# Kernel optimization log

Measured on AMD Instinct MI355X. Metric: run time of the kernel, lower is better.

## Reference

```python
import jax, jax.numpy as jnp
import numpy as np

R, S, H, L = 4096, 64, 256, 3  # rays, samples/ray, mlp width, n hidden-to-hidden layers
FAR_DELTA = 1e10


def setup_inputs() -> dict:
    key = jax.random.key(0)
    ks = jax.random.split(key, 16)
    points = jax.random.normal(ks[0], (R, S, 3), dtype=jnp.float32)
    dirs = jax.random.normal(ks[1], (R, S, 3), dtype=jnp.float32)
    dirs = dirs / jnp.linalg.norm(dirs, axis=-1, keepdims=True)
    # sorted depths in a [2, 6] near/far range (monotone along sample axis)
    z_vals = jnp.sort(2.0 + 4.0 * jax.random.uniform(ks[2], (R, S), dtype=jnp.float32), axis=-1)
    time = jax.random.uniform(ks[3], (R, S), dtype=jnp.float32)

    def w(k, shape):
        return 0.05 * jax.random.normal(k, shape, dtype=jnp.float32)

    return {
        'points': points, 'dirs': dirs, 'z_vals': z_vals, 'time': time,
        'sW_in': w(ks[4], (6, H)),  'sb_in': jnp.zeros((H,), jnp.float32),
        'sW_h':  w(ks[5], (L, H, H)), 'sb_h': jnp.zeros((L, H), jnp.float32),
        'sW_out': w(ks[6], (H, 4)), 'sb_out': jnp.zeros((4,), jnp.float32),
        'dW_in': w(ks[7], (7, H)),  'db_in': jnp.zeros((H,), jnp.float32),
        'dW_h':  w(ks[8], (L, H, H)), 'db_h': jnp.zeros((L, H), jnp.float32),
        'dW_out': w(ks[9], (H, 5)), 'db_out': jnp.zeros((5,), jnp.float32),
    }


def _mlp(x, W_in, b_in, W_h, b_h, W_out, b_out):
    h = jax.nn.relu(x @ W_in + b_in)
    for i in range(W_h.shape[0]):  # fixed small layer count
        h = jax.nn.relu(h @ W_h[i] + b_h[i])
    return h @ W_out + b_out


def _compute_weights(sigma, z_vals):
    delta = z_vals[..., 1:] - z_vals[..., :-1]
    delta = jnp.concatenate([delta, jnp.full_like(delta[..., :1], FAR_DELTA)], axis=-1)
    alpha = 1.0 - jnp.exp(-sigma * delta)
    trans = jnp.cumprod(
        jnp.concatenate([jnp.ones_like(alpha[..., :1]), 1.0 - alpha + 1e-10], axis=-1),
        axis=-1)[..., :-1]
    return alpha * trans


def reference(points, dirs, z_vals, time,
              sW_in, sb_in, sW_h, sb_h, sW_out, sb_out,
              dW_in, db_in, dW_h, db_h, dW_out, db_out):
    static_out = _mlp(jnp.concatenate([points, dirs], axis=-1),
                      sW_in, sb_in, sW_h, sb_h, sW_out, sb_out)          # [R,S,4]
    dynamic_out = _mlp(jnp.concatenate([points, dirs, time[..., None]], axis=-1),
                       dW_in, db_in, dW_h, db_h, dW_out, db_out)         # [R,S,5]

    static_sigma = static_out[..., 0]
    static_rgb = jax.nn.sigmoid(static_out[..., 1:4])
    dynamic_sigma = dynamic_out[..., 0]
    dynamic_rgb = jax.nn.sigmoid(dynamic_out[..., 1:4])
    bw = jax.nn.sigmoid(dynamic_out[..., 4])                             # [R,S]

    sigma = (1.0 - bw) * static_sigma + bw * dynamic_sigma               # [R,S]
    rgb = (1.0 - bw)[..., None] * static_rgb + bw[..., None] * dynamic_rgb  # [R,S,3]

    weights = _compute_weights(sigma, z_vals)                            # [R,S]
    rgb_map = jnp.sum(weights[..., None] * rgb, axis=-2)                 # [R,3]
    depth_map = jnp.sum(weights * z_vals, axis=-1)                       # [R]
    return (rgb_map, depth_map, weights, (1.0 - bw) * weights, bw * weights)
```

## Files before the change

kernel.cpp:

```cpp
#include <hip/hip_runtime.h>

#define R_ 4096
#define S_ 64
#define H_ 256
#define N_ (R_ * S_)
#define FARD 1e10f

typedef __attribute__((ext_vector_type(4))) float f32x4;
typedef __attribute__((ext_vector_type(8))) short short8;
typedef __attribute__((ext_vector_type(8))) int i32x8;

union U8 { short8 s; uint4 u; };
union V8 { i32x8 v; uint4 q[2]; };

__device__ __forceinline__ unsigned int cvt_pk_bf16(float lo, float hi) {
    unsigned int r;
    asm("v_cvt_pk_bf16_f32 %0, %1, %2" : "=v"(r) : "v"(lo), "v"(hi));
    return r;
}
__device__ __forceinline__ unsigned short f2bf(float f) {
    unsigned int x = __float_as_uint(f);
    x += 0x7fffu + ((x >> 16) & 1u);
    return (unsigned short)(x >> 16);
}
__device__ __forceinline__ unsigned int pk4_fp8(float a0, float a1, float a2, float a3) {
    unsigned int lo, hi;
    asm("v_cvt_pk_fp8_f32 %0, %1, %2" : "=v"(lo) : "v"(a0), "v"(a1));
    asm("v_cvt_pk_fp8_f32 %0, %1, %2" : "=v"(hi) : "v"(a2), "v"(a3));
    return (lo & 0xffffu) | (hi << 16);
}
__device__ __forceinline__ unsigned char f2fp8(float v) {
    unsigned int r;
    asm("v_cvt_pk_fp8_f32 %0, %1, %2" : "=v"(r) : "v"(v), "v"(0.0f));
    return (unsigned char)(r & 0xff);
}
__device__ __forceinline__ float sigmoidf_(float x) { return 1.0f / (1.0f + expf(-x)); }

typedef const __attribute__((address_space(1))) unsigned char* gas1;
typedef __attribute__((address_space(3))) unsigned char* las3;
__device__ __forceinline__ void stage64k(const unsigned char* g, unsigned char* l, int tid) {
#pragma unroll
    for (int i = 0; i < 8; ++i)
        __builtin_amdgcn_global_load_lds((gas1)(g + i * 8192 + tid * 16),
                                         (las3)(l + i * 8192 + tid * 16), 16, 0, 0);
}


__device__ __forceinline__ void store_act_frag(unsigned char* act, const unsigned int pk[8],
                                               int lane, int wv)
{
    const int m0 = lane & 15;
    const int q  = lane >> 4;
    const int sp = wv >> 2;
    const int c4 = (wv & 3) << 4;
#pragma unroll
    for (int nt = 0; nt < 2; ++nt)
#pragma unroll
        for (int mt = 0; mt < 4; ++mt)
            *(unsigned int*)(act + (mt * 2 + sp) * 2048 + nt * 1024 +
                             (c4 + m0) * 16 + 4 * q) = pk[nt * 4 + mt];
}

__device__ void hidden_layer(unsigned char* act, unsigned char* wbuf,
                             const unsigned char* __restrict__ next_panel,
                             const float* __restrict__ bias, int lane, int wv, int tid)
{
    const int m0 = lane & 15;
    const int q  = lane >> 4;
    const int nw = wv << 5;

    f32x4 acc[2][4];
#pragma unroll
    for (int nt = 0; nt < 2; ++nt) {
        const float4 bv = *(const float4*)&bias[nw + nt * 16 + 4 * q];
#pragma unroll
        for (int mt = 0; mt < 4; ++mt) {
            acc[nt][mt][0] = bv.x; acc[nt][mt][1] = bv.y;
            acc[nt][mt][2] = bv.z; acc[nt][mt][3] = bv.w;
        }
    }

    __builtin_amdgcn_s_setprio(1);
#pragma unroll
    for (int s = 0; s < 2; ++s) {
        V8 A[2];
#pragma unroll
        for (int nt = 0; nt < 2; ++nt) {
            const int t = wv * 4 + nt * 2 + s;
            A[nt].q[0] = *(const uint4*)(wbuf + t * 2048 + lane * 16);
            A[nt].q[1] = *(const uint4*)(wbuf + t * 2048 + 1024 + lane * 16);
        }
#pragma unroll
        for (int mt = 0; mt < 4; ++mt) {
            V8 B;
            B.q[0] = *(const uint4*)(act + (mt * 2 + s) * 2048 + lane * 16);
            B.q[1] = *(const uint4*)(act + (mt * 2 + s) * 2048 + 1024 + lane * 16);
#pragma unroll
            for (int nt = 0; nt < 2; ++nt)
                acc[nt][mt] = __builtin_amdgcn_mfma_scale_f32_16x16x128_f8f6f4(
                    A[nt].v, B.v, acc[nt][mt], 0, 0,
                    0, 0x7F7F7F7Fu, 0, 0x7F7F7F7Fu);
        }
    }
    __builtin_amdgcn_s_setprio(0);
    __syncthreads();
    if (next_panel) stage64k(next_panel, wbuf, tid);
    unsigned int pk[8];
#pragma unroll
    for (int nt = 0; nt < 2; ++nt)
#pragma unroll
        for (int mt = 0; mt < 4; ++mt) {
            f32x4 a = acc[nt][mt];
            pk[nt * 4 + mt] = pk4_fp8(fmaxf(a[0], 0.f), fmaxf(a[1], 0.f),
                                      fmaxf(a[2], 0.f), fmaxf(a[3], 0.f));
        }
    store_act_frag(act, pk, lane, wv);
    __syncthreads();
}

__device__ void input_compute(const float* __restrict__ pts, const float* __restrict__ drs,
                              const float* __restrict__ tv,
                              const short* __restrict__ WinT, const float* __restrict__ bin,
                              unsigned int pk[8], int base, int lane, int wv)
{
    const int m0 = lane & 15;
    const int q  = lane >> 4;
    const int nw = wv << 5;

    short8 B[4];
#pragma unroll
    for (int mt = 0; mt < 4; ++mt) {
        U8 ub;
        if (q == 0) {
            const int s = base + mt * 16 + m0;
            float p0 = pts[s * 3 + 0], p1 = pts[s * 3 + 1], p2 = pts[s * 3 + 2];
            float e0 = drs[s * 3 + 0], e1 = drs[s * 3 + 1], e2 = drs[s * 3 + 2];
            float t  = tv[s];
            ub.u = make_uint4(cvt_pk_bf16(p0, p1), cvt_pk_bf16(p2, e0),
                              cvt_pk_bf16(e1, e2), cvt_pk_bf16(t, 0.f));
        } else {
            ub.u = make_uint4(0, 0, 0, 0);
        }
        B[mt] = ub.s;
    }

    f32x4 acc[2][4];
#pragma unroll
    for (int nt = 0; nt < 2; ++nt) {
        const float4 bv = *(const float4*)&bin[nw + nt * 16 + 4 * q];
#pragma unroll
        for (int mt = 0; mt < 4; ++mt) {
            acc[nt][mt][0] = bv.x; acc[nt][mt][1] = bv.y;
            acc[nt][mt][2] = bv.z; acc[nt][mt][3] = bv.w;
        }
    }
#pragma unroll
    for (int nt = 0; nt < 2; ++nt) {
        short8 A = *(const short8*)&WinT[(nw + nt * 16 + m0) * 32 + 8 * q];
#pragma unroll
        for (int mt = 0; mt < 4; ++mt)
            acc[nt][mt] = __builtin_amdgcn_mfma_f32_16x16x32_bf16(A, B[mt], acc[nt][mt], 0, 0, 0);
    }
#pragma unroll
    for (int nt = 0; nt < 2; ++nt)
#pragma unroll
        for (int mt = 0; mt < 4; ++mt) {
            f32x4 a = acc[nt][mt];
            pk[nt * 4 + mt] = pk4_fp8(fmaxf(a[0], 0.f), fmaxf(a[1], 0.f),
                                      fmaxf(a[2], 0.f), fmaxf(a[3], 0.f));
        }
}

template <int OUTD>
__device__ void out_mfma(const unsigned char* act, const unsigned char* __restrict__ WoT,
                         const float* __restrict__ bout, float* o, int lane, int wv)
{
    const int q = lane >> 4;

    f32x4 acc = {0.f, 0.f, 0.f, 0.f};
#pragma unroll
    for (int s = 0; s < 2; ++s) {
        V8 A, B;
        A.q[0] = *(const uint4*)(WoT + s * 2048 + lane * 16);
        A.q[1] = *(const uint4*)(WoT + s * 2048 + 1024 + lane * 16);
        B.q[0] = *(const uint4*)(act + (wv * 2 + s) * 2048 + lane * 16);
        B.q[1] = *(const uint4*)(act + (wv * 2 + s) * 2048 + 1024 + lane * 16);
        acc = __builtin_amdgcn_mfma_scale_f32_16x16x128_f8f6f4(
            A.v, B.v, acc, 0, 0, 0, 0x7F7F7F7Fu, 0, 0x7F7F7F7Fu);
    }
    if (q == 0) {
        o[0] = acc[0] + bout[0]; o[1] = acc[1] + bout[1];
        o[2] = acc[2] + bout[2]; o[3] = acc[3] + bout[3];
    }
    if (OUTD == 5 && q == 1) o[4] = acc[0] + bout[4];
}

__global__ __launch_bounds__(512, 4) void nerf_kernel(
    const float* __restrict__ points, const float* __restrict__ dirs,
    const float* __restrict__ z_vals, const float* __restrict__ timev,
    const float* __restrict__ sbin, const float* __restrict__ sbh, const float* __restrict__ sbout,
    const float* __restrict__ dbin, const float* __restrict__ dbh, const float* __restrict__ dbout,
    const unsigned char* __restrict__ wsb,
    float* __restrict__ out)
{
    __shared__ __align__(16) unsigned char wbuf[65536];
    __shared__ __align__(16) unsigned char act[64 * H_];

    const int tid  = threadIdx.x;
    const int lane = tid & 63;
    const int wv   = tid >> 6;
    const int ray  = blockIdx.x;
    const int base = ray * 64;

    const unsigned char* sW8   = wsb;
    const unsigned char* dW8   = wsb + 196608;
    const short* sWinT = (const short*)(wsb + 393216);
    const short* dWinT = (const short*)(wsb + 409600);
    const unsigned char* sWoT8 = wsb + 425984;
    const unsigned char* dWoT8 = wsb + 430080;

    stage64k(sW8 + 0 * 65536, wbuf, tid);
    {
        unsigned int pk[8];
        input_compute(points, dirs, timev, sWinT, sbin, pk, base, lane, wv);
        store_act_frag(act, pk, lane, wv);
    }
    __syncthreads();

    hidden_layer(act, wbuf, sW8 + 1 * 65536, sbh + 0 * H_, lane, wv, tid);
    hidden_layer(act, wbuf, sW8 + 2 * 65536, sbh + 1 * H_, lane, wv, tid);
    hidden_layer(act, wbuf, dW8 + 0 * 65536, sbh + 2 * H_, lane, wv, tid);

    float so[4];
    unsigned int dpk[8];
    input_compute(points, dirs, timev, dWinT, dbin, dpk, base, lane, wv);
    if (wv < 4) out_mfma<4>(act, sWoT8, sbout, so, lane, wv);
    __syncthreads();
    store_act_frag(act, dpk, lane, wv);
    __syncthreads();

    hidden_layer(act, wbuf, dW8 + 1 * 65536, dbh + 0 * H_, lane, wv, tid);
    hidden_layer(act, wbuf, dW8 + 2 * 65536, dbh + 1 * H_, lane, wv, tid);
    hidden_layer(act, wbuf, nullptr,         dbh + 2 * H_, lane, wv, tid);

    float dox[5];
    if (wv < 4) out_mfma<5>(act, dWoT8, dbout, dox, lane, wv);
    __syncthreads();

    float* mixb = (float*)act;
    if (wv < 4) {
        const int m0 = lane & 15;
        const int q  = lane >> 4;
        const int m  = (wv << 4) + m0;
        if (q == 0) {
            mixb[m * 9 + 0] = so[0];  mixb[m * 9 + 1] = so[1];
            mixb[m * 9 + 2] = so[2];  mixb[m * 9 + 3] = so[3];
            mixb[m * 9 + 4] = dox[0]; mixb[m * 9 + 5] = dox[1];
            mixb[m * 9 + 6] = dox[2]; mixb[m * 9 + 7] = dox[3];
        }
        if (q == 1) mixb[m * 9 + 8] = dox[4];
    }
    __syncthreads();

    if (tid < 64) {
        const int s = tid;
        float so0 = mixb[s * 9 + 0], so1 = mixb[s * 9 + 1];
        float so2 = mixb[s * 9 + 2], so3 = mixb[s * 9 + 3];
        float d0 = mixb[s * 9 + 4], d1 = mixb[s * 9 + 5], d2 = mixb[s * 9 + 6];
        float d3 = mixb[s * 9 + 7], d4 = mixb[s * 9 + 8];

        float bw  = sigmoidf_(d4);
        float omb = 1.f - bw;
        float sigma = omb * so0 + bw * d0;
        float cr = omb * sigmoidf_(so1) + bw * sigmoidf_(d1);
        float cg = omb * sigmoidf_(so2) + bw * sigmoidf_(d2);
        float cb = omb * sigmoidf_(so3) + bw * sigmoidf_(d3);

        float z  = z_vals[base + s];
        float zn = __shfl_down(z, 1);
        float delta = (s < 63) ? (zn - z) : FARD;
        float ex    = fminf(-sigma * delta, 60.0f);
        float alpha = 1.f - expf(ex);
        float f     = 1.f - alpha + 1e-10f;
        float p = f;
#pragma unroll
        for (int d = 1; d < 64; d <<= 1) {
            float pu = __shfl_up(p, d);
            if (s >= d) p *= pu;
        }
        float T = (s == 0) ? 1.f : __shfl_up(p, 1);
        float w = alpha * T;

        float* rgb_map   = out;
        float* depth_map = out + R_ * 3;
        float* weights   = out + R_ * 4;
        float* swei      = weights + N_;
        float* dwei      = swei + N_;
        weights[base + s] = w;
        swei[base + s]    = omb * w;
        dwei[base + s]    = bw * w;

        float c0 = w * cr, c1 = w * cg, c2 = w * cb, dd = w * z;
#pragma unroll
        for (int d = 32; d >= 1; d >>= 1) {
            c0 += __shfl_down(c0, d);
            c1 += __shfl_down(c1, d);
            c2 += __shfl_down(c2, d);
            dd += __shfl_down(dd, d);
        }
        if (s == 0) {
            rgb_map[ray * 3 + 0] = c0;
            rgb_map[ray * 3 + 1] = c1;
            rgb_map[ray * 3 + 2] = c2;
            depth_map[ray] = dd;
        }
    }
}

__global__ void convert_weights(const float* __restrict__ sWh, const float* __restrict__ dWh,
                                const float* __restrict__ sWin, const float* __restrict__ dWin,
                                const float* __restrict__ sWout, const float* __restrict__ dWout,
                                unsigned char* __restrict__ ws)
{
    int idx = blockIdx.x * 256 + threadIdx.x;
    if (idx < 393216) {
        int which = idx >= 196608;
        int rem   = which ? idx - 196608 : idx;
        int l = rem >> 16, e = rem & 65535;
        int t = e >> 11, r2 = e & 2047;
        int h = r2 >> 10, r3 = r2 & 1023;
        int ln = r3 >> 4, b = r3 & 15;
        int wv = t >> 2, nt = (t >> 1) & 1, s = t & 1;
        int n = wv * 32 + nt * 16 + (ln & 15);
        int k = s * 128 + (ln >> 4) * 32 + h * 16 + b;
        const float* W = which ? dWh : sWh;
        ws[idx] = f2fp8(W[l * 65536 + k * 256 + n]);
    } else if (idx < 409600) {
        int j = idx - 393216;
        int which = j >= 8192;
        int e = j & 8191;
        int n = e >> 5, k = e & 31;
        int ink = which ? 7 : 6;
        const float* W = which ? dWin : sWin;
        float v = (k < ink) ? W[k * 256 + n] : 0.f;
        ((short*)(ws + 393216))[j] = (short)f2bf(v);
    } else {
        int j = idx - 409600;
        int which = j >= 4096;
        int e = j & 4095;
        int s = e >> 11, r2 = e & 2047;
        int h = r2 >> 10, r3 = r2 & 1023;
        int ln = r3 >> 4, b = r3 & 15;
        int o = ln & 15;
        int k = s * 128 + (ln >> 4) * 32 + h * 16 + b;
        int outd = which ? 5 : 4;
        const float* W = which ? dWout : sWout;
        float v = (o < outd) ? W[k * outd + o] : 0.f;
        ws[425984 + (which ? 4096 : 0) + e] = f2fp8(v);
    }
}

extern "C" void kernel_launch(void* const* d_in, const int* in_sizes, int n_in,
                              void* d_out, int out_size, void* d_ws, size_t ws_size,
                              hipStream_t stream)
{
    const float* points = (const float*)d_in[0];
    const float* dirs   = (const float*)d_in[1];
    const float* z_vals = (const float*)d_in[2];
    const float* timev  = (const float*)d_in[3];
    const float* sWin   = (const float*)d_in[4];
    const float* sbin   = (const float*)d_in[5];
    const float* sWh    = (const float*)d_in[6];
    const float* sbh    = (const float*)d_in[7];
    const float* sWout  = (const float*)d_in[8];
    const float* sbout  = (const float*)d_in[9];
    const float* dWin   = (const float*)d_in[10];
    const float* dbin   = (const float*)d_in[11];
    const float* dWh    = (const float*)d_in[12];
    const float* dbh    = (const float*)d_in[13];
    const float* dWout  = (const float*)d_in[14];
    const float* dbout  = (const float*)d_in[15];

    unsigned char* wsb = (unsigned char*)d_ws;

    convert_weights<<<1632, 256, 0, stream>>>(sWh, dWh, sWin, dWin, sWout, dWout, wsb);

    nerf_kernel<<<R_, 512, 0, stream>>>(
        points, dirs, z_vals, timev,
        sbin, sbh, sbout, dbin, dbh, dbout,
        wsb, (float*)d_out);
}
```

Before: 158.8 us.

## Process two rays per block and double-buffer weight panels in LDS

Each block now handles two rays (128 samples) with 1024 threads. Two groups of eight waves share each staged 64KB weight panel, which halves the weight staging traffic per ray. The weight buffer is split into two 64KB halves, and the next layer's panel is prefetched at the start of each layer so its load overlaps the MFMA work. Shared memory use rises to about 160KB per block, so at most one block fits per CU. The larger block also means more threads wait at each barrier.

Result: slower. 167.6 us (+5.5%).

```diff
diff --git a/kernel.cpp b/kernel.cpp
--- a/kernel.cpp
+++ b/kernel.cpp
@@ -40,34 +40,35 @@
 typedef __attribute__((address_space(3))) unsigned char* las3;
 __device__ __forceinline__ void stage64k(const unsigned char* g, unsigned char* l, int tid) {
 #pragma unroll
-    for (int i = 0; i < 8; ++i)
-        __builtin_amdgcn_global_load_lds((gas1)(g + i * 8192 + tid * 16),
-                                         (las3)(l + i * 8192 + tid * 16), 16, 0, 0);
-}
-
+    for (int i = 0; i < 4; ++i)
+        __builtin_amdgcn_global_load_lds((gas1)(g + i * 16384 + tid * 16),
+                                         (las3)(l + i * 16384 + tid * 16), 16, 0, 0);
+}
 
 __device__ __forceinline__ void store_act_frag(unsigned char* act, const unsigned int pk[8],
-                                               int lane, int wv)
+                                               int lane, int wq, int sh)
 {
     const int m0 = lane & 15;
     const int q  = lane >> 4;
-    const int sp = wv >> 2;
-    const int c4 = (wv & 3) << 4;
+    const int sp = wq >> 2;
+    const int c4 = (wq & 3) << 4;
 #pragma unroll
     for (int nt = 0; nt < 2; ++nt)
 #pragma unroll
         for (int mt = 0; mt < 4; ++mt)
-            *(unsigned int*)(act + (mt * 2 + sp) * 2048 + nt * 1024 +
+            *(unsigned int*)(act + ((sh * 4 + mt) * 2 + sp) * 2048 + nt * 1024 +
                              (c4 + m0) * 16 + 4 * q) = pk[nt * 4 + mt];
 }
 
-__device__ void hidden_layer(unsigned char* act, unsigned char* wbuf,
+__device__ void hidden_layer(unsigned char* act, unsigned char* wcur, unsigned char* wnext,
                              const unsigned char* __restrict__ next_panel,
-                             const float* __restrict__ bias, int lane, int wv, int tid)
+                             const float* __restrict__ bias, int lane, int wq, int sh, int tid)
 {
     const int m0 = lane & 15;
     const int q  = lane >> 4;
-    const int nw = wv << 5;
+    const int nw = wq << 5;
+
+    if (next_panel) stage64k(next_panel, wnext, tid);
 
     f32x4 acc[2][4];
 #pragma unroll
@@ -86,15 +87,16 @@
         V8 A[2];
 #pragma unroll
         for (int nt = 0; nt < 2; ++nt) {
-            const int t = wv * 4 + nt * 2 + s;
-            A[nt].q[0] = *(const uint4*)(wbuf + t * 2048 + lane * 16);
-            A[nt].q[1] = *(const uint4*)(wbuf + t * 2048 + 1024 + lane * 16);
+            const int t = wq * 4 + nt * 2 + s;
+            A[nt].q[0] = *(const uint4*)(wcur + t * 2048 + lane * 16);
+            A[nt].q[1] = *(const uint4*)(wcur + t * 2048 + 1024 + lane * 16);
         }
 #pragma unroll
         for (int mt = 0; mt < 4; ++mt) {
             V8 B;
-            B.q[0] = *(const uint4*)(act + (mt * 2 + s) * 2048 + lane * 16);
-            B.q[1] = *(const uint4*)(act + (mt * 2 + s) * 2048 + 1024 + lane * 16);
+            const int bt = ((sh * 4 + mt) * 2 + s) * 2048;
+            B.q[0] = *(const uint4*)(act + bt + lane * 16);
+            B.q[1] = *(const uint4*)(act + bt + 1024 + lane * 16);
 #pragma unroll
             for (int nt = 0; nt < 2; ++nt)
                 acc[nt][mt] = __builtin_amdgcn_mfma_scale_f32_16x16x128_f8f6f4(
@@ -104,7 +106,6 @@
     }
     __builtin_amdgcn_s_setprio(0);
     __syncthreads();
-    if (next_panel) stage64k(next_panel, wbuf, tid);
     unsigned int pk[8];
 #pragma unroll
     for (int nt = 0; nt < 2; ++nt)
@@ -114,25 +115,25 @@
             pk[nt * 4 + mt] = pk4_fp8(fmaxf(a[0], 0.f), fmaxf(a[1], 0.f),
                                       fmaxf(a[2], 0.f), fmaxf(a[3], 0.f));
         }
-    store_act_frag(act, pk, lane, wv);
+    store_act_frag(act, pk, lane, wq, sh);
     __syncthreads();
 }
 
 __device__ void input_compute(const float* __restrict__ pts, const float* __restrict__ drs,
                               const float* __restrict__ tv,
                               const short* __restrict__ WinT, const float* __restrict__ bin,
-                              unsigned int pk[8], int base, int lane, int wv)
+                              unsigned int pk[8], int base, int lane, int wq, int sh)
 {
     const int m0 = lane & 15;
     const int q  = lane >> 4;
-    const int nw = wv << 5;
+    const int nw = wq << 5;
 
     short8 B[4];
 #pragma unroll
     for (int mt = 0; mt < 4; ++mt) {
         U8 ub;
         if (q == 0) {
-            const int s = base + mt * 16 + m0;
+            const int s = base + sh * 64 + mt * 16 + m0;
             float p0 = pts[s * 3 + 0], p1 = pts[s * 3 + 1], p2 = pts[s * 3 + 2];
             float e0 = drs[s * 3 + 0], e1 = drs[s * 3 + 1], e2 = drs[s * 3 + 2];
             float t  = tv[s];
@@ -195,7 +196,7 @@
     if (OUTD == 5 && q == 1) o[4] = acc[0] + bout[4];
 }
 
-__global__ __launch_bounds__(512, 4) void nerf_kernel(
+__global__ __launch_bounds__(1024, 4) void nerf_kernel(
     const float* __restrict__ points, const float* __restrict__ dirs,
     const float* __restrict__ z_vals, const float* __restrict__ timev,
     const float* __restrict__ sbin, const float* __restrict__ sbh, const float* __restrict__ sbout,
@@ -203,14 +204,16 @@
     const unsigned char* __restrict__ wsb,
     float* __restrict__ out)
 {
-    __shared__ __align__(16) unsigned char wbuf[65536];
-    __shared__ __align__(16) unsigned char act[64 * H_];
+    __shared__ __align__(16) unsigned char wbuf0[65536];
+    __shared__ __align__(16) unsigned char wbuf1[65536];
+    __shared__ __align__(16) unsigned char act[32768];
 
     const int tid  = threadIdx.x;
     const int lane = tid & 63;
     const int wv   = tid >> 6;
-    const int ray  = blockIdx.x;
-    const int base = ray * 64;
+    const int wq   = wv & 7;
+    const int sh   = wv >> 3;
+    const int base = blockIdx.x * 128;
 
     const unsigned char* sW8   = wsb;
     const unsigned char* dW8   = wsb + 196608;
@@ -219,39 +222,39 @@
     const unsigned char* sWoT8 = wsb + 425984;
     const unsigned char* dWoT8 = wsb + 430080;
 
-    stage64k(sW8 + 0 * 65536, wbuf, tid);
+    stage64k(sW8 + 0 * 65536, wbuf0, tid);
     {
         unsigned int pk[8];
-        input_compute(points, dirs, timev, sWinT, sbin, pk, base, lane, wv);
-        store_act_frag(act, pk, lane, wv);
-    }
-    __syncthreads();
-
-    hidden_layer(act, wbuf, sW8 + 1 * 65536, sbh + 0 * H_, lane, wv, tid);
-    hidden_layer(act, wbuf, sW8 + 2 * 65536, sbh + 1 * H_, lane, wv, tid);
-    hidden_layer(act, wbuf, dW8 + 0 * 65536, sbh + 2 * H_, lane, wv, tid);
+        input_compute(points, dirs, timev, sWinT, sbin, pk, base, lane, wq, sh);
+        store_act_frag(act, pk, lane, wq, sh);
+    }
+    __syncthreads();
+
+    hidden_layer(act, wbuf0, wbuf1, sW8 + 1 * 65536, sbh + 0 * H_, lane, wq, sh, tid);
+    hidden_layer(act, wbuf1, wbuf0, sW8 + 2 * 65536, sbh + 1 * H_, lane, wq, sh, tid);
+    hidden_layer(act, wbuf0, wbuf1, dW8 + 0 * 65536, sbh + 2 * H_, lane, wq, sh, tid);
 
     float so[4];
     unsigned int dpk[8];
-    input_compute(points, dirs, timev, dWinT, dbin, dpk, base, lane, wv);
-    if (wv < 4) out_mfma<4>(act, sWoT8, sbout, so, lane, wv);
-    __syncthreads();
-    store_act_frag(act, dpk, lane, wv);
-    __syncthreads();
-
-    hidden_layer(act, wbuf, dW8 + 1 * 65536, dbh + 0 * H_, lane, wv, tid);
-    hidden_layer(act, wbuf, dW8 + 2 * 65536, dbh + 1 * H_, lane, wv, tid);
-    hidden_layer(act, wbuf, nullptr,         dbh + 2 * H_, lane, wv, tid);
+    input_compute(points, dirs, timev, dWinT, dbin, dpk, base, lane, wq, sh);
+    if (wv < 8) out_mfma<4>(act, sWoT8, sbout, so, lane, wv);
+    __syncthreads();
+    store_act_frag(act, dpk, lane, wq, sh);
+    __syncthreads();
+
+    hidden_layer(act, wbuf1, wbuf0, dW8 + 1 * 65536, dbh + 0 * H_, lane, wq, sh, tid);
+    hidden_layer(act, wbuf0, wbuf1, dW8 + 2 * 65536, dbh + 1 * H_, lane, wq, sh, tid);
+    hidden_layer(act, wbuf1, wbuf0, nullptr,         dbh + 2 * H_, lane, wq, sh, tid);
 
     float dox[5];
-    if (wv < 4) out_mfma<5>(act, dWoT8, dbout, dox, lane, wv);
+    if (wv < 8) out_mfma<5>(act, dWoT8, dbout, dox, lane, wv);
     __syncthreads();
 
     float* mixb = (float*)act;
-    if (wv < 4) {
+    if (wv < 8) {
         const int m0 = lane & 15;
         const int q  = lane >> 4;
-        const int m  = (wv << 4) + m0;
+        const int m  = wv * 16 + m0;
         if (q == 0) {
             mixb[m * 9 + 0] = so[0];  mixb[m * 9 + 1] = so[1];
             mixb[m * 9 + 2] = so[2];  mixb[m * 9 + 3] = so[3];
@@ -262,12 +265,13 @@
     }
     __syncthreads();
 
-    if (tid < 64) {
-        const int s = tid;
-        float so0 = mixb[s * 9 + 0], so1 = mixb[s * 9 + 1];
-        float so2 = mixb[s * 9 + 2], so3 = mixb[s * 9 + 3];
-        float d0 = mixb[s * 9 + 4], d1 = mixb[s * 9 + 5], d2 = mixb[s * 9 + 6];
-        float d3 = mixb[s * 9 + 7], d4 = mixb[s * 9 + 8];
+    if (tid < 128) {
+        const int sl  = tid & 63;
+        const int ray = blockIdx.x * 2 + (tid >> 6);
+        float so0 = mixb[tid * 9 + 0], so1 = mixb[tid * 9 + 1];
+        float so2 = mixb[tid * 9 + 2], so3 = mixb[tid * 9 + 3];
+        float d0 = mixb[tid * 9 + 4], d1 = mixb[tid * 9 + 5], d2 = mixb[tid * 9 + 6];
+        float d3 = mixb[tid * 9 + 7], d4 = mixb[tid * 9 + 8];
 
         float bw  = sigmoidf_(d4);
         float omb = 1.f - bw;
@@ -276,9 +280,9 @@
         float cg = omb * sigmoidf_(so2) + bw * sigmoidf_(d2);
         float cb = omb * sigmoidf_(so3) + bw * sigmoidf_(d3);
 
-        float z  = z_vals[base + s];
+        float z  = z_vals[base + tid];
         float zn = __shfl_down(z, 1);
-        float delta = (s < 63) ? (zn - z) : FARD;
+        float delta = (sl < 63) ? (zn - z) : FARD;
         float ex    = fminf(-sigma * delta, 60.0f);
         float alpha = 1.f - expf(ex);
         float f     = 1.f - alpha + 1e-10f;
@@ -286,9 +290,9 @@
 #pragma unroll
         for (int d = 1; d < 64; d <<= 1) {
             float pu = __shfl_up(p, d);
-            if (s >= d) p *= pu;
-        }
-        float T = (s == 0) ? 1.f : __shfl_up(p, 1);
+            if (sl >= d) p *= pu;
+        }
+        float T = (sl == 0) ? 1.f : __shfl_up(p, 1);
         float w = alpha * T;
 
         float* rgb_map   = out;
@@ -296,9 +300,9 @@
         float* weights   = out + R_ * 4;
         float* swei      = weights + N_;
         float* dwei      = swei + N_;
-        weights[base + s] = w;
-        swei[base + s]    = omb * w;
-        dwei[base + s]    = bw * w;
+        weights[base + tid] = w;
+        swei[base + tid]    = omb * w;
+        dwei[base + tid]    = bw * w;
 
         float c0 = w * cr, c1 = w * cg, c2 = w * cb, dd = w * z;
 #pragma unroll
@@ -308,7 +312,7 @@
             c2 += __shfl_down(c2, d);
             dd += __shfl_down(dd, d);
         }
-        if (s == 0) {
+        if (sl == 0) {
             rgb_map[ray * 3 + 0] = c0;
             rgb_map[ray * 3 + 1] = c1;
             rgb_map[ray * 3 + 2] = c2;
@@ -385,7 +389,7 @@
 
     convert_weights<<<1632, 256, 0, stream>>>(sWh, dWh, sWin, dWin, sWout, dWout, wsb);
 
-    nerf_kernel<<<R_, 512, 0, stream>>>(
+    nerf_kernel<<<R_ / 2, 1024, 0, stream>>>(
         points, dirs, z_vals, timev,
         sbin, sbh, sbout, dbin, dbh, dbout,
         wsb, (float*)d_out);
```
